# Performance work log

Hardware: AMD Instinct MI355X
Metric: run time of the kernel (lower is better)

## Reference

```python
import jax, jax.numpy as jnp
import numpy as np
from jax import lax

_OFFS = [(dx, dy, dz) for dx in (-1, 0, 1) for dy in (-1, 0, 1) for dz in (-1, 0, 1)]


def _cell(coords, S):
    # padded linear cell index: spatial dims get +1 shift into an (S+2)^3 grid so
    # +/-1 neighbor offsets never leave the slab
    P = S + 2
    return ((coords[:, 0] * P + coords[:, 1] + 1) * P + coords[:, 2] + 1) * P + coords[:, 3] + 1


def _build_grid(coords, S, n_slabs):
    g = jnp.full((n_slabs * (S + 2) ** 3,), -1, jnp.int32)
    return g.at[_cell(coords, S)].set(jnp.arange(coords.shape[0], dtype=jnp.int32))


def _forward(voxel_coords, voxel_feats, centroid_scores, offsets, bg_desc, W_desc, mixer_W, mixer_b, S, B):
    N, C = voxel_feats.shape
    TAU, PEAK_THRESH, K = 0.1, 0.2, 128
    # ---------- _revoxelize (torch: @no_grad) ----------
    off4 = jnp.concatenate([jnp.zeros((N, 1), jnp.int32), offsets.astype(jnp.int32)], 1)
    new_coords = voxel_coords + off4
    key = _cell(new_coords, S)                       # sphash equivalent (coords are unique per cell)
    order = jnp.argsort(key)
    ks = key[order]
    newflag = jnp.concatenate([jnp.ones((1,), bool), ks[1:] != ks[:-1]])
    sid = jnp.cumsum(newflag.astype(jnp.int32)) - 1
    seg = jnp.zeros((N,), jnp.int32).at[order].set(sid)      # idx_query (unique -> fixed N segments)
    counts = jax.ops.segment_sum(jnp.ones((N,), jnp.float32), seg, num_segments=N)
    mean_coords = jax.ops.segment_sum(new_coords.astype(jnp.float32), seg, num_segments=N) / jnp.maximum(counts, 1.0)[:, None]
    clus_coords = mean_coords.astype(jnp.int32)              # spvoxelize(...).int()
    valid_clus = counts > 0
    clus_coords = clus_coords.at[:, 0].set(jnp.where(valid_clus, clus_coords[:, 0], B))  # park empty segs in spare slab
    cpv = counts[seg][:, None]                                # counts gathered per voxel
    clus_sum = jax.ops.segment_sum(voxel_feats / cpv, seg, num_segments=N)  # scatter_sum(F/counts)
    # submanifold 3x3x3 avg pool over cluster sites
    cgrid = _build_grid(clus_coords, S, B + 1)
    acc = jnp.zeros_like(clus_sum)
    cnt = jnp.zeros((N, 1), jnp.float32)
    for off in _OFFS:
        nc = clus_coords + jnp.array([0, *off], jnp.int32)
        j = cgrid[_cell(nc, S)]
        v = (j >= 0)[:, None]
        acc = acc + jnp.where(v, clus_sum[jnp.maximum(j, 0)], 0.0)
        cnt = cnt + v.astype(jnp.float32)
    pooled = acc / jnp.maximum(cnt, 1.0)
    cluster_feats = lax.stop_gradient(pooled[seg])            # [N, C], gathered back per voxel
    cluster_scores = lax.stop_gradient(cpv)                   # [N, 1]
    # ---------- union + mixer 3x3x3 subm conv ----------
    vgrid = _build_grid(voxel_coords, S, B)
    featsAB = jnp.concatenate([centroid_scores, cluster_scores], 1)  # same coords -> hash union is identity match
    mix = jnp.broadcast_to(mixer_b, (N, 1)).astype(jnp.float32)
    for kth, off in enumerate(_OFFS):
        nc = voxel_coords + jnp.array([0, *off], jnp.int32)
        j = vgrid[_cell(nc, S)]
        v = (j >= 0)[:, None]
        mix = mix + jnp.where(v, featsAB[jnp.maximum(j, 0)] @ mixer_W[kth], 0.0)
    refined = jax.nn.sigmoid(mix)                             # [N, 1]
    # ---------- _find_centroid_peaks (torch: @no_grad), NMS via subm max-pool ----------
    score = lax.stop_gradient(refined[:, 0])
    m = score > TAU
    val = jnp.where(m, score, -jnp.inf)                       # submanifold active set = masked voxels
    hmax = jnp.full((N,), -jnp.inf, jnp.float32)
    for off in _OFFS:
        nc = voxel_coords + jnp.array([0, *off], jnp.int32)
        j = vgrid[_cell(nc, S)]
        nv = jnp.where(j >= 0, val[jnp.maximum(j, 0)], -jnp.inf)
        hmax = jnp.maximum(hmax, nv)
    peak = m & (hmax == score) & (score > PEAK_THRESH)
    top_vals, top_idx = lax.top_k(jnp.where(peak, score, -1.0), K)
    valid_peak = top_vals > 0.0
    conf = jnp.where(valid_peak, top_vals, 0.0)[:, None]      # [K, 1]
    peak_feats = jnp.where(valid_peak[:, None], cluster_feats[top_idx], 0.0)
    # ---------- descriptors + instance logits ----------
    voxel_desc = jax.nn.relu(cluster_feats @ W_desc)          # 1x1x1 sparse conv + ReLU == pointwise linear
    peak_desc = conf * jax.nn.relu(peak_feats @ W_desc)       # [K, D]
    descriptors = jnp.concatenate([bg_desc, peak_desc], 0)    # [K+1, D]
    instance = (voxel_desc @ descriptors.T)[seg]              # gather-matmul then index_select(inv_map)
    return refined, conf, instance


def setup_inputs() -> dict:
    rng = np.random.default_rng(0)
    S, B, N = 96, 2, 200000
    LATENT, DESC = 64, 32
    C = LATENT + 3
    inner = S - 8  # keep coords in [4, S-5] so coords + offsets in [-4,4] stay in-bounds
    per = N // B
    coords = []
    for b in range(B):
        lin = rng.choice(inner ** 3, size=per, replace=False)  # unique voxel coords per batch
        x = lin // (inner * inner)
        y = (lin // inner) % inner
        z = lin % inner
        coords.append(np.stack([np.full(per, b), x + 4, y + 4, z + 4], 1))
    coords = jnp.asarray(np.concatenate(coords, 0).astype(np.int32))
    ks = jax.random.split(jax.random.key(0), 8)
    return dict(
        voxel_coords=coords,
        voxel_feats=jax.random.normal(ks[0], (N, C), jnp.float32),
        centroid_scores=jax.random.uniform(ks[1], (N, 1), dtype=jnp.float32),
        offsets=jax.random.randint(ks[2], (N, 3), -4, 5).astype(jnp.float32),
        bg_desc=jax.random.normal(ks[3], (1, DESC), jnp.float32) * 0.02,
        W_desc=jax.random.normal(ks[4], (C, DESC), jnp.float32) * 0.05,
        mixer_W=jax.random.normal(ks[5], (27, 2, 1), jnp.float32) * 0.5,
        mixer_b=jnp.zeros((1,), jnp.float32),
        spatial_size=S,
        batch_size=B,
    )


def reference(voxel_coords, voxel_feats, centroid_scores, offsets, bg_desc, W_desc, mixer_W, mixer_b, spatial_size, batch_size):
    return _forward(voxel_coords, voxel_feats, centroid_scores, offsets, bg_desc, W_desc, mixer_W, mixer_b, int(spatial_size), int(batch_size))
```

## Files before the change

### kernel.cpp

```cpp
#include <hip/hip_runtime.h>
#include <stdint.h>

#define S_   96
#define P_   98
#define NB_  2
#define GSZ  (NB_*P_*P_*P_)
#define C_   67
#define CP_  68
#define D_   32
#define KTOP 128
#define SELCAP 1024

typedef unsigned int u32;
typedef unsigned long long u64;

struct Ctrl {
  u64 prefix;
  int n_peaks;
  int kk;
  int selctr;
  int nseg;
};

__device__ __forceinline__ int cell4(int b, int x, int y, int z) {
  return ((b*P_ + x + 1)*P_ + y + 1)*P_ + z + 1;
}

__global__ __launch_bounds__(256) void k_clear(int4* __restrict__ rank, int4* __restrict__ cgrid,
                                               int4* __restrict__ vgrid, int4* __restrict__ cnts, int N) {
  const int R4 = GSZ/4;
  const int N4 = N/4;
  int idx = blockIdx.x*256 + threadIdx.x;
  int stride = gridDim.x*256;
  const int4 z = make_int4(0,0,0,0), m1 = make_int4(-1,-1,-1,-1);
  for (int i = idx; i < R4; i += stride) { rank[i] = z; cgrid[i] = m1; vgrid[i] = m1; }
  for (int i = idx; i < N4; i += stride) cnts[i] = z;
}

__global__ __launch_bounds__(1024) void k_init(Ctrl* c, int* __restrict__ hist) {
  int t = threadIdx.x;
  for (int i = t; i < 65536; i += 1024) hist[i] = 0;
  if (t == 0) { c->prefix = 0ull; c->n_peaks = 0; c->kk = KTOP; c->selctr = 0; }
}

__global__ __launch_bounds__(256) void k_key(const int* __restrict__ vc, const float* __restrict__ offs,
                                             int* __restrict__ keyA, int* __restrict__ rank,
                                             int* __restrict__ vgrid, int N) {
  int i = blockIdx.x*256 + threadIdx.x;
  if (i >= N) return;
  const int4 q = ((const int4*)vc)[i];
  int ox = (int)offs[3*i], oy = (int)offs[3*i+1], oz = (int)offs[3*i+2];
  int k = cell4(q.x, q.y+ox, q.z+oy, q.w+oz);
  keyA[i] = k;
  rank[k] = 1;
  vgrid[cell4(q.x, q.y, q.z, q.w)] = i;
}

#define SC_TPB 256
#define SC_EPT 8
#define SC_EPB (SC_TPB*SC_EPT)

__global__ __launch_bounds__(SC_TPB) void k_scan1(int* __restrict__ a, int* __restrict__ bsum, int n) {
  __shared__ int sd[SC_TPB];
  int t = threadIdx.x;
  int base = blockIdx.x*SC_EPB + t*SC_EPT;
  int x[SC_EPT]; int s = 0;
  #pragma unroll
  for (int e = 0; e < SC_EPT; ++e) { int idx = base+e; x[e] = (idx < n) ? a[idx] : 0; s += x[e]; }
  sd[t] = s; __syncthreads();
  for (int off = 1; off < SC_TPB; off <<= 1) {
    int v = (t >= off) ? sd[t-off] : 0; __syncthreads(); sd[t] += v; __syncthreads();
  }
  int run = sd[t] - s;
  #pragma unroll
  for (int e = 0; e < SC_EPT; ++e) { int idx = base+e; if (idx < n) a[idx] = run; run += x[e]; }
  if (t == SC_TPB-1) bsum[blockIdx.x] = sd[t];
}

__global__ __launch_bounds__(SC_TPB) void k_scan2(int* __restrict__ bsum, int nb, Ctrl* ctrl) {
  __shared__ int sd[SC_TPB];
  int t = threadIdx.x;
  int x[4]; int s = 0;
  #pragma unroll
  for (int e = 0; e < 4; ++e) { int idx = t*4+e; x[e] = (idx < nb) ? bsum[idx] : 0; s += x[e]; }
  sd[t] = s; __syncthreads();
  for (int off = 1; off < SC_TPB; off <<= 1) {
    int v = (t >= off) ? sd[t-off] : 0; __syncthreads(); sd[t] += v; __syncthreads();
  }
  int run = sd[t] - s;
  #pragma unroll
  for (int e = 0; e < 4; ++e) { int idx = t*4+e; if (idx < nb) bsum[idx] = run; run += x[e]; }
  if (t == SC_TPB-1) ctrl->nseg = sd[t];
}

__global__ __launch_bounds__(SC_TPB) void k_scan3(int* __restrict__ a, const int* __restrict__ bsum, int n) {
  int add = bsum[blockIdx.x];
  int base = blockIdx.x*SC_EPB + threadIdx.x*SC_EPT;
  #pragma unroll
  for (int e = 0; e < SC_EPT; ++e) { int idx = base+e; if (idx < n) a[idx] += add; }
}

__global__ __launch_bounds__(256) void k_seg(const int* __restrict__ keyA, const int* __restrict__ rank,
                                             int* __restrict__ seg, int* __restrict__ cnts,
                                             int* __restrict__ cgrid, int* __restrict__ ckey, int N) {
  int i = blockIdx.x*256 + threadIdx.x;
  if (i >= N) return;
  int k = keyA[i];
  int s = rank[k];
  seg[i] = s;
  atomicAdd(&cnts[s], 1);
  cgrid[k] = s;
  ckey[s] = k;
}

__global__ __launch_bounds__(256) void k_fabzero(const int* __restrict__ seg, const int* __restrict__ cnts,
                                                 const float* __restrict__ cent, float2* __restrict__ fab,
                                                 int* __restrict__ g2, float* __restrict__ clussum, int N) {
  int i = blockIdx.x*256 + threadIdx.x;
  if (i >= N) return;
  int s = seg[i];
  int c = cnts[s];
  fab[i] = make_float2(cent[i], (float)c);
  g2[i] = seg[s];
  if (c > 1) {
    float4* row = (float4*)(clussum + (size_t)s*CP_);
    const float4 fz = make_float4(0.f,0.f,0.f,0.f);
    #pragma unroll
    for (int k = 0; k < CP_/4; ++k) row[k] = fz;
  }
}

__global__ __launch_bounds__(256) void k_accum(const int* __restrict__ seg, const int* __restrict__ cnts,
                                               const float* __restrict__ feats,
                                               float* __restrict__ clussum, int N) {
  int t = threadIdx.x;
  int i = blockIdx.x*4 + (t >> 6);
  if (i >= N) return;
  int lane = t & 63;
  int s = seg[i];
  int cnt = cnts[s];
  float inv = 1.0f/(float)cnt;
  const float* fr = feats + (size_t)i*C_;
  float* dst = clussum + (size_t)s*CP_;
  float v0 = fr[lane]*inv;
  float v1 = (lane < C_-64) ? fr[64+lane]*inv : 0.f;
  if (cnt == 1) {
    dst[lane] = v0;
    if (lane < C_-64) dst[64+lane] = v1;
  } else {
    atomicAdd(&dst[lane], v0);
    if (lane < C_-64) atomicAdd(&dst[64+lane], v1);
  }
}

__global__ __launch_bounds__(64) void k_pool(const Ctrl* __restrict__ ctrl,
                                             const int* __restrict__ ckey, const int* __restrict__ cgrid,
                                             const float* __restrict__ clussum, const float* __restrict__ Wd,
                                             float* __restrict__ V) {
  int nseg = ctrl->nseg;
  int s0 = blockIdx.x*2;
  if (s0 >= nseg) return;
  int t = threadIdx.x;
  int half = t >> 5, l = t & 31;
  int s = s0 + half;
  bool segok = (s < nseg);
  int j = -1;
  if (segok && l < 27) {
    int dx = l/9 - 1, dy = (l/3)%3 - 1, dz = l%3 - 1;
    j = cgrid[ckey[s] + (dx*P_ + dy)*P_ + dz];
  }
  float a0 = 0.f, a1 = 0.f, b0 = 0.f, b1 = 0.f;
  int nva = 0, nvb = 0;
  #pragma unroll
  for (int k = 0; k < 27; ++k) {
    int ja = __shfl(j, k);
    int jb = __shfl(j, 32 + k);
    if (ja >= 0) {
      const float* r = clussum + (size_t)ja*CP_;
      a0 += r[t];
      if (t < 3) a1 += r[64 + t];
      ++nva;
    }
    if (jb >= 0) {
      const float* r = clussum + (size_t)jb*CP_;
      b0 += r[t];
      if (t < 3) b1 += r[64 + t];
      ++nvb;
    }
  }
  __shared__ float pL[2][CP_];
  float inva = 1.f/(float)(nva > 0 ? nva : 1);
  pL[0][t] = a0*inva;
  if (t < 3) pL[0][64 + t] = a1*inva;
  if (s0 + 1 < nseg) {
    float invb = 1.f/(float)(nvb > 0 ? nvb : 1);
    pL[1][t] = b0*invb;
    if (t < 3) pL[1][64 + t] = b1*invb;
  }
  __syncthreads();
  if (segok) {
    const float* p = pL[half];
    float acc = 0.f;
    #pragma unroll
    for (int c = 0; c < C_; ++c) acc += p[c] * Wd[c*D_ + l];
    V[(size_t)s*D_ + l] = fmaxf(acc, 0.f);
  }
}

__global__ __launch_bounds__(256) void k_mixer(const int* __restrict__ vc, const int* __restrict__ vgrid,
                                               const float2* __restrict__ fab, const float* __restrict__ mW,
                                               const float* __restrict__ mB, float* __restrict__ out, int N) {
  int i = blockIdx.x*256 + threadIdx.x;
  if (i >= N) return;
  const int4 q = ((const int4*)vc)[i];
  int bc = cell4(q.x, q.y, q.z, q.w);
  float mix = mB[0];
  #pragma unroll
  for (int k = 0; k < 27; ++k) {
    int dx = k/9 - 1, dy = (k/3)%3 - 1, dz = k%3 - 1;
    int j = vgrid[bc + (dx*P_ + dy)*P_ + dz];
    int jc = (j >= 0) ? j : 0;
    float2 f = fab[jc];
    float msk = (j >= 0) ? 1.f : 0.f;
    mix += msk * (f.x*mW[2*k] + f.y*mW[2*k+1]);
  }
  out[i] = 1.f/(1.f + expf(-mix));
}

__global__ __launch_bounds__(256) void k_peak(const int* __restrict__ vc, const int* __restrict__ vgrid,
                                              const float* __restrict__ out, Ctrl* __restrict__ ctrl,
                                              u64* __restrict__ cand, int N) {
  int i = blockIdx.x*256 + threadIdx.x;
  if (i >= N) return;
  const float NINF = __int_as_float(0xff800000);
  float sc = out[i];
  const int4 q = ((const int4*)vc)[i];
  int bc = cell4(q.x, q.y, q.z, q.w);
  float hmax = NINF;
  #pragma unroll
  for (int k = 0; k < 27; ++k) {
    int dx = k/9 - 1, dy = (k/3)%3 - 1, dz = k%3 - 1;
    int j = vgrid[bc + (dx*P_ + dy)*P_ + dz];
    int jc = (j >= 0) ? j : 0;
    float sj = out[jc];
    float vj = (j >= 0 && sj > 0.1f) ? sj : NINF;
    hmax = fmaxf(hmax, vj);
  }
  if (sc > 0.2f && hmax == sc) {
    int pos = atomicAdd(&ctrl->n_peaks, 1);
    cand[pos] = ((u64)__float_as_uint(sc) << 32) | (u32)(~(u32)i);
  }
}

__global__ __launch_bounds__(256) void k_hist(const u64* __restrict__ cand, const Ctrl* __restrict__ ctrl,
                                              int* __restrict__ hist, int shift) {
  int idx = blockIdx.x*256 + threadIdx.x;
  if (idx >= ctrl->n_peaks) return;
  u64 key = cand[idx];
  if (shift != 48 && (((key ^ ctrl->prefix) >> (shift + 16)) != 0)) return;
  atomicAdd(&hist[(int)((key >> shift) & 0xFFFF)], 1);
}

__global__ __launch_bounds__(1024) void k_scansel(int* __restrict__ hist, Ctrl* __restrict__ ctrl, int shift) {
  __shared__ int sd[1024];
  int t = threadIdx.x;
  int kk = ctrl->kk;
  int lo = 65536 - (t+1)*64;
  int s = 0;
  for (int b = lo; b < lo+64; ++b) s += hist[b];
  sd[t] = s; __syncthreads();
  for (int off = 1; off < 1024; off <<= 1) {
    int v = (t >= off) ? sd[t-off] : 0; __syncthreads(); sd[t] += v; __syncthreads();
  }
  int before = sd[t] - s;
  if (before < kk && before + s >= kk) {
    int cum = before;
    for (int b = lo+63; b >= lo; --b) {
      int h = hist[b];
      if (cum + h >= kk) { ctrl->prefix |= ((u64)(u32)b) << shift; ctrl->kk = kk - cum; break; }
      cum += h;
    }
  }
  __syncthreads();
  for (int b = lo; b < lo+64; ++b) hist[b] = 0;
}

__global__ __launch_bounds__(256) void k_collect(const u64* __restrict__ cand, Ctrl* __restrict__ ctrl,
                                                 u64* __restrict__ sel) {
  int idx = blockIdx.x*256 + threadIdx.x;
  int np = ctrl->n_peaks;
  if (idx >= np) return;
  u64 key = cand[idx];
  bool take = (np <= KTOP) ? true : ((u32)(key >> 32) >= (u32)(ctrl->prefix >> 32));
  if (take) { int pos = atomicAdd(&ctrl->selctr, 1); if (pos < SELCAP) sel[pos] = key; }
}

__global__ __launch_bounds__(SELCAP) void k_rank(const u64* __restrict__ sel, const Ctrl* __restrict__ ctrl,
                                                 float* __restrict__ out, int* __restrict__ topidx, int N) {
  __shared__ u64 sk[SELCAP];
  int t = threadIdx.x;
  int ns = ctrl->selctr; if (ns > SELCAP) ns = SELCAP;
  if (t < KTOP) { out[N + t] = 0.f; topidx[t] = -1; }
  sk[t] = (t < ns) ? sel[t] : 0ull;
  __syncthreads();
  if (t < ns) {
    u64 my = sk[t];
    int r = 0;
    for (int m = 0; m < ns; ++m) r += (sk[m] > my) ? 1 : 0;
    if (r < KTOP) {
      out[N + r] = __uint_as_float((u32)(my >> 32));
      topidx[r]  = (int)~(u32)(my & 0xFFFFFFFFull);
    }
  }
}

__global__ void k_desc(const int* __restrict__ topidx, const int* __restrict__ seg,
                       const float* __restrict__ V, const float* __restrict__ bg,
                       const float* __restrict__ outc, float* __restrict__ descg, int N) {
  int b = blockIdx.x; int d = threadIdx.x;
  if (b == 0) { descg[d] = bg[d]; return; }
  int r = b - 1;
  int ti = topidx[r];
  float v = 0.f;
  if (ti >= 0) v = outc[N + r] * V[(size_t)seg[ti]*D_ + d];
  descg[b*D_ + d] = v;
}

#define VPB 128
__global__ __launch_bounds__(256) void k_inst(const int* __restrict__ g2, const float* __restrict__ V,
                                              const float* __restrict__ descg, float* __restrict__ out, int N) {
  __shared__ __align__(16) float dsT[32*136];
  __shared__ __align__(16) float ds128[32];
  __shared__ __align__(16) float us[VPB*D_];
  __shared__ int gs[VPB];
  int tid = threadIdx.x;
  for (int idx = tid; idx < 128*D_; idx += 256) {
    int d = idx >> 7, cc = idx & 127;
    dsT[d*136 + ((cc & 31) << 2) + (cc >> 5)] = descg[cc*D_ + d];
  }
  if (tid < 32) ds128[tid] = descg[128*D_ + tid];
  int v0 = blockIdx.x*VPB;
  if (tid < VPB) { int v = v0 + tid; gs[tid] = (v < N) ? g2[v] : -1; }
  __syncthreads();
  for (int idx = tid; idx < VPB*D_; idx += 256) {
    int v = idx >> 5, d = idx & 31; int g = gs[v];
    us[idx] = (g >= 0) ? V[(size_t)g*D_ + d] : 0.f;
  }
  __syncthreads();
  int hw = tid >> 5, tx = tid & 31;
  #pragma unroll 1
  for (int s = 0; s < 4; ++s) {
    int vb = s*32 + hw*4;
    float4 acc[4];
    #pragma unroll
    for (int k = 0; k < 4; ++k) acc[k] = make_float4(0.f,0.f,0.f,0.f);
    float a128[4] = {0.f, 0.f, 0.f, 0.f};
    #pragma unroll 2
    for (int d4 = 0; d4 < 8; ++d4) {
      float4 uv[4];
      #pragma unroll
      for (int k = 0; k < 4; ++k) uv[k] = *(const float4*)(us + (vb+k)*D_ + d4*4);
      #pragma unroll
      for (int dd = 0; dd < 4; ++dd) {
        float4 dv = *(const float4*)(dsT + (size_t)(d4*4+dd)*136 + tx*4);
        #pragma unroll
        for (int k = 0; k < 4; ++k) {
          float u = (dd==0) ? uv[k].x : (dd==1) ? uv[k].y : (dd==2) ? uv[k].z : uv[k].w;
          acc[k].x += u*dv.x; acc[k].y += u*dv.y; acc[k].z += u*dv.z; acc[k].w += u*dv.w;
        }
      }
      if (tx == 0) {
        float4 e = *(const float4*)(ds128 + d4*4);
        #pragma unroll
        for (int k = 0; k < 4; ++k)
          a128[k] += uv[k].x*e.x + uv[k].y*e.y + uv[k].z*e.z + uv[k].w*e.w;
      }
    }
    #pragma unroll
    for (int k = 0; k < 4; ++k) {
      int gv = v0 + vb + k;
      if (gv < N) {
        float* o = out + (size_t)gv*129;
        o[tx]      = acc[k].x;
        o[tx + 32] = acc[k].y;
        o[tx + 64] = acc[k].z;
        o[tx + 96] = acc[k].w;
        if (tx == 0) o[128] = a128[k];
      }
    }
  }
}

extern "C" void kernel_launch(void* const* d_in, const int* in_sizes, int n_in,
                              void* d_out, int out_size, void* d_ws, size_t ws_size,
                              hipStream_t stream) {
  const int*   vc    = (const int*)d_in[0];
  const float* feats = (const float*)d_in[1];
  const float* cent  = (const float*)d_in[2];
  const float* offs  = (const float*)d_in[3];
  const float* bg    = (const float*)d_in[4];
  const float* Wd    = (const float*)d_in[5];
  const float* mW    = (const float*)d_in[6];
  const float* mB    = (const float*)d_in[7];
  int N = in_sizes[2];

  float* out = (float*)d_out;

  uint8_t* base = (uint8_t*)d_ws;
  size_t off = 0;
  auto carve = [&](size_t bytes) -> void* {
    off = (off + 255) & ~(size_t)255;
    void* r = base + off; off += bytes; return r;
  };
  Ctrl*   ctrl    = (Ctrl*)  carve(sizeof(Ctrl));
  int*    keyA    = (int*)   carve((size_t)N*4);
  int*    seg     = (int*)   carve((size_t)N*4);
  int*    cnts    = (int*)   carve((size_t)N*4);
  int*    ckey    = (int*)   carve((size_t)N*4);
  int*    g2      = (int*)   carve((size_t)N*4);
  float2* fab     = (float2*)carve((size_t)N*8);
  int*    rank    = (int*)   carve((size_t)GSZ*4);
  int*    bsum    = (int*)   carve(1024*4);
  int*    cgrid   = (int*)   carve((size_t)GSZ*4);
  int*    vgrid   = (int*)   carve((size_t)GSZ*4);
  float*  clussum = (float*) carve((size_t)N*CP_*4);
  float*  V       = (float*) carve((size_t)N*D_*4);
  u64*    cand    = (u64*)   carve((size_t)N*8);
  int*    hist    = (int*)   carve(65536*4);
  u64*    sel     = (u64*)   carve(SELCAP*8);
  int*    topidx  = (int*)   carve(KTOP*4);
  float*  descg   = (float*) carve(129*D_*4);

  int nb256 = (N + 255)/256;
  int nscan = (GSZ + SC_EPB - 1)/SC_EPB;
  int nclr  = (GSZ/4 + 255)/256;

  k_clear<<<nclr, 256, 0, stream>>>((int4*)rank, (int4*)cgrid, (int4*)vgrid, (int4*)cnts, N);
  k_init<<<1, 1024, 0, stream>>>(ctrl, hist);

  k_key<<<nb256, 256, 0, stream>>>(vc, offs, keyA, rank, vgrid, N);
  k_scan1<<<nscan, SC_TPB, 0, stream>>>(rank, bsum, GSZ);
  k_scan2<<<1, SC_TPB, 0, stream>>>(bsum, nscan, ctrl);
  k_scan3<<<nscan, SC_TPB, 0, stream>>>(rank, bsum, GSZ);
  k_seg<<<nb256, 256, 0, stream>>>(keyA, rank, seg, cnts, cgrid, ckey, N);

  k_fabzero<<<nb256, 256, 0, stream>>>(seg, cnts, cent, fab, g2, clussum, N);
  k_accum<<<(N + 3)/4, 256, 0, stream>>>(seg, cnts, feats, clussum, N);
  k_pool<<<(N + 1)/2, 64, 0, stream>>>(ctrl, ckey, cgrid, clussum, Wd, V);

  k_mixer<<<nb256, 256, 0, stream>>>(vc, vgrid, fab, mW, mB, out, N);
  k_peak<<<nb256, 256, 0, stream>>>(vc, vgrid, out, ctrl, cand, N);

  for (int shift = 48; shift >= 32; shift -= 16) {
    k_hist<<<nb256, 256, 0, stream>>>(cand, ctrl, hist, shift);
    k_scansel<<<1, 1024, 0, stream>>>(hist, ctrl, shift);
  }
  k_collect<<<nb256, 256, 0, stream>>>(cand, ctrl, sel);
  k_rank<<<1, SELCAP, 0, stream>>>(sel, ctrl, out, topidx, N);

  k_desc<<<KTOP + 1, D_, 0, stream>>>(topidx, seg, V, bg, out, descg, N);
  k_inst<<<(N + VPB - 1)/VPB, 256, 0, stream>>>(g2, V, descg, out + N + KTOP, N);
}
```

Before: 615.2 us.

## Batch neighbor loads in k_pool and remap workgroups across XCDs

The 27-neighbor gather loop in k_pool now issues nine unconditional loads at a time (invalid neighbors are redirected to row 0) and only masks the accumulation, using a ballot to count valid neighbors. The branchy, serialized load-then-add chain should become batches of independent memory requests with more loads in flight. Block indices are also remapped so consecutive segment pairs land on the same XCD, aiming for better L2 locality between neighboring segments. The cost is extra loads for empty neighbors and more registers per thread.

```diff
diff --git a/kernel.cpp b/kernel.cpp
--- a/kernel.cpp
+++ b/kernel.cpp
@@ -158,7 +158,11 @@
                                              const float* __restrict__ clussum, const float* __restrict__ Wd,
                                              float* __restrict__ V) {
   int nseg = ctrl->nseg;
-  int s0 = blockIdx.x*2;
+  int nwg = gridDim.x;
+  int q = nwg >> 3, rr = nwg & 7;
+  int xcd = blockIdx.x & 7, sub = blockIdx.x >> 3;
+  int wg = (xcd < rr ? xcd*(q+1) : rr*(q+1) + (xcd - rr)*q) + sub;
+  int s0 = wg*2;
   if (s0 >= nseg) return;
   int t = threadIdx.x;
   int half = t >> 5, l = t & 31;
@@ -169,23 +173,28 @@
     int dx = l/9 - 1, dy = (l/3)%3 - 1, dz = l%3 - 1;
     j = cgrid[ckey[s] + (dx*P_ + dy)*P_ + dz];
   }
+  u64 mk = __ballot(j >= 0);
+  int nva = (int)__popcll(mk & 0x7FFFFFFull);
+  int nvb = (int)__popcll((mk >> 32) & 0x7FFFFFFull);
+  int js = (j < 0) ? 0 : j;
   float a0 = 0.f, a1 = 0.f, b0 = 0.f, b1 = 0.f;
-  int nva = 0, nvb = 0;
-  #pragma unroll
-  for (int k = 0; k < 27; ++k) {
-    int ja = __shfl(j, k);
-    int jb = __shfl(j, 32 + k);
-    if (ja >= 0) {
-      const float* r = clussum + (size_t)ja*CP_;
-      a0 += r[t];
-      if (t < 3) a1 += r[64 + t];
-      ++nva;
-    }
-    if (jb >= 0) {
-      const float* r = clussum + (size_t)jb*CP_;
-      b0 += r[t];
-      if (t < 3) b1 += r[64 + t];
-      ++nvb;
+  int t4 = 64 + (t & 3);
+  #pragma unroll 1
+  for (int g = 0; g < 27; g += 9) {
+    float ra[9], sa[9], rb[9], sb[9];
+    #pragma unroll
+    for (int k = 0; k < 9; ++k) {
+      int ja = __shfl(js, g + k);
+      int jb = __shfl(js, 32 + g + k);
+      const float* rA = clussum + (size_t)ja*CP_;
+      const float* rB = clussum + (size_t)jb*CP_;
+      ra[k] = rA[t];  sa[k] = rA[t4];
+      rb[k] = rB[t];  sb[k] = rB[t4];
+    }
+    #pragma unroll
+    for (int k = 0; k < 9; ++k) {
+      if ((mk >> (g + k)) & 1ull)      { a0 += ra[k]; a1 += sa[k]; }
+      if ((mk >> (32 + g + k)) & 1ull) { b0 += rb[k]; b1 += sb[k]; }
     }
   }
   __shared__ float pL[2][CP_];
```

Result: slower. 647.5 us (+5.3%).
